# Kernel optimization log

Hardware: AMD Instinct MI355X
Metric: run time of the kernel (lower is better)

## Reference

```python
import jax, jax.numpy as jnp
import numpy as np

S, N, H = 1024, 64, 1024  # source len, batch, hidden_size
INPUT_SIZE = 1024         # attention projection dim (linear1/linear2 out)


def setup_inputs() -> dict:
    key = jax.random.key(0)
    ks = jax.random.split(key, 8)
    sc_h = 1.0 / np.sqrt(H)
    sc_i = 1.0 / np.sqrt(INPUT_SIZE)
    return {
        "out_e": jax.random.normal(ks[0], (S, N, H), dtype=jnp.float32),
        "hidden_d": jax.random.normal(ks[1], (1, N, H), dtype=jnp.float32),
        # torch Linear weights are [out_features, in_features]
        "W1": jax.random.uniform(ks[2], (INPUT_SIZE, H), jnp.float32, -sc_h, sc_h),
        "b1": jax.random.uniform(ks[3], (INPUT_SIZE,), jnp.float32, -sc_h, sc_h),
        "W2": jax.random.uniform(ks[4], (INPUT_SIZE, H), jnp.float32, -sc_h, sc_h),
        "b2": jax.random.uniform(ks[5], (INPUT_SIZE,), jnp.float32, -sc_h, sc_h),
        "W3": jax.random.uniform(ks[6], (1, INPUT_SIZE), jnp.float32, -sc_i, sc_i),
        "b3": jax.random.uniform(ks[7], (1,), jnp.float32, -sc_i, sc_i),
    }


def reference(out_e, hidden_d, W1, b1, W2, b2, W3, b3):
    # hidden_d [1,N,H] broadcast to [S,N,H] (torch .repeat)
    s = out_e.shape[0]
    hd = jnp.broadcast_to(hidden_d, (s,) + hidden_d.shape[1:])
    # a: [S,N,1] = linear3(tanh(linear1(hd) + linear2(out_e)))
    e = jnp.tanh(hd @ W1.T + b1 + out_e @ W2.T + b2)
    a = e @ W3.T + b3
    # softmax over the source dim (dim=0 in torch)
    alpha = jax.nn.softmax(a, axis=0)          # [S,N,1]
    c = jnp.einsum('sne,snh->enh', alpha, out_e)  # [1,N,H]
    return (c, alpha)
```

## Files before the change

### kernel.cpp

```cpp
#include <hip/hip_runtime.h>
#include <hip/hip_fp16.h>

#define S_LEN 1024
#define N_B   64
#define H_DIM 1024
#define I_DIM 1024

typedef __attribute__((ext_vector_type(8))) _Float16 half8;
typedef __attribute__((ext_vector_type(4))) _Float16 half4;
typedef __attribute__((ext_vector_type(4))) float    f32x4;

__device__ __forceinline__ void gload16(const void* g, void* l) {
  __builtin_amdgcn_global_load_lds(
      (const __attribute__((address_space(1))) unsigned int*)g,
      (__attribute__((address_space(3))) unsigned int*)l, 16, 0, 0);
}

__global__ __launch_bounds__(256) void setup_kernel(
    const float* __restrict__ out_e, const float* __restrict__ hd,
    const float* __restrict__ W1, const float* __restrict__ b1,
    const float* __restrict__ b2, const float* __restrict__ W2,
    _Float16* __restrict__ oe16, _Float16* __restrict__ w216,
    float* __restrict__ u1, float* __restrict__ a_ws,
    float* __restrict__ c_out) {
  __shared__ float hs[4 * 1024];
  const int bx = blockIdx.x;
  const int t = threadIdx.x;

  if (bx < 4096) {
    const float4* s4 = (const float4*)out_e;
    half8* d8 = (half8*)oe16;
    int i = bx * 256 + t;
#pragma unroll
    for (int r = 0; r < 8; ++r, i += 1048576) {
      float4 a = s4[2 * i], b = s4[2 * i + 1];
      half8 h;
      h[0] = (_Float16)a.x; h[1] = (_Float16)a.y;
      h[2] = (_Float16)a.z; h[3] = (_Float16)a.w;
      h[4] = (_Float16)b.x; h[5] = (_Float16)b.y;
      h[6] = (_Float16)b.z; h[7] = (_Float16)b.w;
      d8[i] = h;
    }
    return;
  }
  if (bx < 4160) {
    const float4* s4 = (const float4*)W2;
    half8* d8 = (half8*)w216;
    int i = (bx - 4096) * 256 + t;
#pragma unroll
    for (int r = 0; r < 8; ++r, i += 16384) {
      float4 a = s4[2 * i], b = s4[2 * i + 1];
      half8 h;
      h[0] = (_Float16)a.x; h[1] = (_Float16)a.y;
      h[2] = (_Float16)a.z; h[3] = (_Float16)a.w;
      h[4] = (_Float16)b.x; h[5] = (_Float16)b.y;
      h[6] = (_Float16)b.z; h[7] = (_Float16)b.w;
      d8[i] = h;
    }
    return;
  }
  const int local = bx - 4160;
  a_ws[local * 256 + t] = 0.f;
  c_out[local * 256 + t] = 0.f;

  const int nb = local & 15;
  const int ib = local >> 4;
  const int n0 = nb * 4;

  const float4* g4 = (const float4*)(hd + (size_t)n0 * 1024);
  float4* h4 = (float4*)hs;
#pragma unroll
  for (int r = 0; r < 4; ++r) h4[r * 256 + t] = g4[r * 256 + t];
  __syncthreads();

  int il = t >> 2, q = t & 3;
  int i = ib * 64 + il;
  const float4* w4 = (const float4*)(W1 + (size_t)i * 1024 + q * 256);
  float s0 = 0.f, s1 = 0.f, s2 = 0.f, s3 = 0.f;
  for (int hh = 0; hh < 64; ++hh) {
    float4 wv = w4[hh];
    int hb = q * 256 + hh * 4;
    float4 v0 = *(const float4*)&hs[0 * 1024 + hb];
    float4 v1 = *(const float4*)&hs[1 * 1024 + hb];
    float4 v2 = *(const float4*)&hs[2 * 1024 + hb];
    float4 v3 = *(const float4*)&hs[3 * 1024 + hb];
    s0 += wv.x * v0.x + wv.y * v0.y + wv.z * v0.z + wv.w * v0.w;
    s1 += wv.x * v1.x + wv.y * v1.y + wv.z * v1.z + wv.w * v1.w;
    s2 += wv.x * v2.x + wv.y * v2.y + wv.z * v2.z + wv.w * v2.w;
    s3 += wv.x * v3.x + wv.y * v3.y + wv.z * v3.z + wv.w * v3.w;
  }
  s0 += __shfl_xor(s0, 1); s0 += __shfl_xor(s0, 2);
  s1 += __shfl_xor(s1, 1); s1 += __shfl_xor(s1, 2);
  s2 += __shfl_xor(s2, 1); s2 += __shfl_xor(s2, 2);
  s3 += __shfl_xor(s3, 1); s3 += __shfl_xor(s3, 2);
  if (q == 0) {
    float bb = b1[i] + b2[i];
    u1[(size_t)(n0 + 0) * 1024 + i] = s0 + bb;
    u1[(size_t)(n0 + 1) * 1024 + i] = s1 + bb;
    u1[(size_t)(n0 + 2) * 1024 + i] = s2 + bb;
    u1[(size_t)(n0 + 3) * 1024 + i] = s3 + bb;
  }
}

__global__ __launch_bounds__(256) void fused_gemm_tanh(
    const _Float16* __restrict__ A,
    const _Float16* __restrict__ B,
    const float* __restrict__ u1,
    const float* __restrict__ W3,
    float* __restrict__ a_ws)
{
  __shared__ __align__(16) _Float16 As[2][128 * 32];
  __shared__ __align__(16) _Float16 Bs[2][128 * 32];

  const int t = threadIdx.x;
  const int lane = t & 63;
  const int w = t >> 6;
  const int wr = w >> 1, wc = w & 1;
  const int bx = blockIdx.x;
  const int xcd = bx & 7;
  const int j = bx >> 3;
  const int rb = xcd + ((j >> 3) << 3);
  const int cb = j & 7;
  const int m0 = rb * 128, i0 = cb * 128;

  const int strow = t >> 2;
  const int stcol = (t & 3) * 8;
  const _Float16* gA = A + (size_t)(m0 + strow) * 1024 + stcol;
  const _Float16* gB = B + (size_t)(i0 + strow) * 1024 + stcol;
  const int ldsoff = strow * 32 + stcol;

  f32x4 acc[4][4] = {};

  gload16(gA,             &As[0][ldsoff]);
  gload16(gA + 64 * 1024, &As[0][ldsoff + 64 * 32]);
  gload16(gB,             &Bs[0][ldsoff]);
  gload16(gB + 64 * 1024, &Bs[0][ldsoff + 64 * 32]);
  __syncthreads();

  const int fr = lane & 15;
  const int kg = lane >> 4;
  const int aoff = (wr * 64 + fr) * 32 + kg * 8;
  const int boff = (wc * 64 + fr) * 32 + kg * 8;

  for (int kt = 0; kt < 32; ++kt) {
    const int buf = kt & 1;
    if (kt < 31) {
      const _Float16* gA2 = gA + (kt + 1) * 32;
      const _Float16* gB2 = gB + (kt + 1) * 32;
      gload16(gA2,             &As[buf ^ 1][ldsoff]);
      gload16(gA2 + 64 * 1024, &As[buf ^ 1][ldsoff + 64 * 32]);
      gload16(gB2,             &Bs[buf ^ 1][ldsoff]);
      gload16(gB2 + 64 * 1024, &Bs[buf ^ 1][ldsoff + 64 * 32]);
    }
    half8 af[4], bf[4];
#pragma unroll
    for (int mi = 0; mi < 4; ++mi)
      af[mi] = *(const half8*)&As[buf][aoff + mi * 16 * 32];
#pragma unroll
    for (int ni = 0; ni < 4; ++ni)
      bf[ni] = *(const half8*)&Bs[buf][boff + ni * 16 * 32];
#pragma unroll
    for (int mi = 0; mi < 4; ++mi)
#pragma unroll
      for (int ni = 0; ni < 4; ++ni)
        acc[mi][ni] = __builtin_amdgcn_mfma_f32_16x16x32_f16(
            af[mi], bf[ni], acc[mi][ni], 0, 0, 0);
    __syncthreads();
  }

  float w3v[4];
#pragma unroll
  for (int ni = 0; ni < 4; ++ni)
    w3v[ni] = W3[i0 + wc * 64 + ni * 16 + fr];

#pragma unroll
  for (int mi = 0; mi < 4; ++mi) {
#pragma unroll
    for (int jj = 0; jj < 4; ++jj) {
      int m = m0 + wr * 64 + mi * 16 + kg * 4 + jj;
      int n = m & 63;
      const float* u1row = u1 + (size_t)n * 1024 + i0 + wc * 64;
      float s = 0.f;
#pragma unroll
      for (int ni = 0; ni < 4; ++ni) {
        float e = acc[mi][ni][jj] + u1row[ni * 16 + fr];
        float th = 1.f - 2.f / (__expf(2.f * e) + 1.f);
        s += th * w3v[ni];
      }
      s += __shfl_xor(s, 1);
      s += __shfl_xor(s, 2);
      s += __shfl_xor(s, 4);
      s += __shfl_xor(s, 8);
      if (fr == 0) atomicAdd(&a_ws[m], s);
    }
  }
}

__global__ __launch_bounds__(256) void softmax_wsum(
    const float* __restrict__ a_ws, const _Float16* __restrict__ oe,
    float* __restrict__ alpha, float* __restrict__ cout) {
  const int n = blockIdx.x & 63;
  const int sc = blockIdx.x >> 6;
  const int t = threadIdx.x;
  __shared__ float red[256];
  __shared__ float al[64];

  float v[4];
  float mx = -1e30f;
#pragma unroll
  for (int q = 0; q < 4; ++q) {
    v[q] = a_ws[(size_t)(t + q * 256) * 64 + n];
    mx = fmaxf(mx, v[q]);
  }
  red[t] = mx; __syncthreads();
  for (int off = 128; off > 0; off >>= 1) {
    if (t < off) red[t] = fmaxf(red[t], red[t + off]);
    __syncthreads();
  }
  mx = red[0];
  __syncthreads();
  float sum = 0.f;
#pragma unroll
  for (int q = 0; q < 4; ++q) { v[q] = __expf(v[q] - mx); sum += v[q]; }
  red[t] = sum; __syncthreads();
  for (int off = 128; off > 0; off >>= 1) {
    if (t < off) red[t] += red[t + off];
    __syncthreads();
  }
  const float inv = 1.f / red[0];

  const int q0 = sc >> 2;
  const int tlo = (sc & 3) * 64;
  if (t >= tlo && t < tlo + 64) {
    float a = v[q0] * inv;
    al[t - tlo] = a;
    alpha[(size_t)(sc * 64 + (t - tlo)) * 64 + n] = a;
  }
  __syncthreads();

  float a0 = 0.f, a1 = 0.f, a2 = 0.f, a3 = 0.f;
#pragma unroll 4
  for (int sl = 0; sl < 64; ++sl) {
    float a = al[sl];
    int s = sc * 64 + sl;
    half4 x = *(const half4*)(oe + (size_t)(s * 64 + n) * 1024 + t * 4);
    a0 += a * (float)x[0]; a1 += a * (float)x[1];
    a2 += a * (float)x[2]; a3 += a * (float)x[3];
  }
  float* c = cout + (size_t)n * 1024 + t * 4;
  atomicAdd(c + 0, a0);
  atomicAdd(c + 1, a1);
  atomicAdd(c + 2, a2);
  atomicAdd(c + 3, a3);
}

extern "C" void kernel_launch(void* const* d_in, const int* in_sizes, int n_in,
                              void* d_out, int out_size, void* d_ws,
                              size_t ws_size, hipStream_t stream) {
  const float* out_e    = (const float*)d_in[0];
  const float* hidden_d = (const float*)d_in[1];
  const float* W1       = (const float*)d_in[2];
  const float* b1       = (const float*)d_in[3];
  const float* W2       = (const float*)d_in[4];
  const float* b2       = (const float*)d_in[5];
  const float* W3       = (const float*)d_in[6];

  char* ws = (char*)d_ws;
  _Float16* oe16 = (_Float16*)ws;
  _Float16* w216 = (_Float16*)(ws + 134217728);
  float* u1   = (float*)(ws + 134217728 + 2097152);
  float* a_ws = (float*)(ws + 134217728 + 2097152 + 262144);

  float* c_out = (float*)d_out;
  float* alpha = (float*)d_out + 65536;

  hipLaunchKernelGGL(setup_kernel, dim3(4416), dim3(256), 0, stream,
                     out_e, hidden_d, W1, b1, b2, W2,
                     oe16, w216, u1, a_ws, c_out);
  hipLaunchKernelGGL(fused_gemm_tanh, dim3(4096), dim3(256), 0, stream,
                     oe16, w216, u1, W3, a_ws);
  hipLaunchKernelGGL(softmax_wsum, dim3(1024), dim3(256), 0, stream,
                     a_ws, oe16, alpha, c_out);
}
```

Baseline: 648.4 us.

## Enlarge GEMM tiles to 256x256 with 4-stage LDS pipeline and priority scheduling

```diff
diff --git a/kernel.cpp b/kernel.cpp
--- a/kernel.cpp
+++ b/kernel.cpp
@@ -102,88 +102,105 @@
   }
 }
 
-__global__ __launch_bounds__(256) void fused_gemm_tanh(
+__global__ __launch_bounds__(512, 2) void fused_gemm_tanh(
     const _Float16* __restrict__ A,
     const _Float16* __restrict__ B,
     const float* __restrict__ u1,
     const float* __restrict__ W3,
     float* __restrict__ a_ws)
 {
-  __shared__ __align__(16) _Float16 As[2][128 * 32];
-  __shared__ __align__(16) _Float16 Bs[2][128 * 32];
+  __shared__ __align__(16) _Float16 As[4][256 * 32];
+  __shared__ __align__(16) _Float16 Bs[4][256 * 32];
 
   const int t = threadIdx.x;
   const int lane = t & 63;
   const int w = t >> 6;
-  const int wr = w >> 1, wc = w & 1;
+  const int wr = w >> 2, wc = w & 3;
   const int bx = blockIdx.x;
   const int xcd = bx & 7;
   const int j = bx >> 3;
-  const int rb = xcd + ((j >> 3) << 3);
-  const int cb = j & 7;
-  const int m0 = rb * 128, i0 = cb * 128;
-
-  const int strow = t >> 2;
-  const int stcol = (t & 3) * 8;
-  const _Float16* gA = A + (size_t)(m0 + strow) * 1024 + stcol;
-  const _Float16* gB = B + (size_t)(i0 + strow) * 1024 + stcol;
-  const int ldsoff = strow * 32 + stcol;
-
-  f32x4 acc[4][4] = {};
-
-  gload16(gA,             &As[0][ldsoff]);
-  gload16(gA + 64 * 1024, &As[0][ldsoff + 64 * 32]);
-  gload16(gB,             &Bs[0][ldsoff]);
-  gload16(gB + 64 * 1024, &Bs[0][ldsoff + 64 * 32]);
-  __syncthreads();
+  const int rb = xcd + ((j >> 2) << 3);
+  const int cb = j & 3;
+  const int m0 = rb * 256, i0 = cb * 256;
 
   const int fr = lane & 15;
   const int kg = lane >> 4;
-  const int aoff = (wr * 64 + fr) * 32 + kg * 8;
+
+  const _Float16* gA0 = A + (size_t)(m0 + (t >> 2)) * 1024 + (t & 3) * 8;
+  const _Float16* gB0 = B + (size_t)(i0 + (t >> 2)) * 1024 + (t & 3) * 8;
+  const int ldst = t * 8;
+
+#define STAGE_A(kt) do { int b_ = (kt) & 3; int kc = (kt) * 32;      \
+    gload16(gA0 + kc,          &As[b_][ldst]);                        \
+    gload16(gA0 + kc + 131072, &As[b_][ldst + 4096]); } while (0)
+#define STAGE_B(kt) do { int b_ = (kt) & 3; int kc = (kt) * 32;      \
+    gload16(gB0 + kc,          &Bs[b_][ldst]);                        \
+    gload16(gB0 + kc + 131072, &Bs[b_][ldst + 4096]); } while (0)
+
+  f32x4 acc[8][4] = {};
+
+  STAGE_A(0); STAGE_B(0);
+  STAGE_A(1); STAGE_B(1);
+  STAGE_A(2); STAGE_B(2);
+
+  const int aoff = (wr * 128 + fr) * 32 + kg * 8;
   const int boff = (wc * 64 + fr) * 32 + kg * 8;
 
-  for (int kt = 0; kt < 32; ++kt) {
-    const int buf = kt & 1;
-    if (kt < 31) {
-      const _Float16* gA2 = gA + (kt + 1) * 32;
-      const _Float16* gB2 = gB + (kt + 1) * 32;
-      gload16(gA2,             &As[buf ^ 1][ldsoff]);
-      gload16(gA2 + 64 * 1024, &As[buf ^ 1][ldsoff + 64 * 32]);
-      gload16(gB2,             &Bs[buf ^ 1][ldsoff]);
-      gload16(gB2 + 64 * 1024, &Bs[buf ^ 1][ldsoff + 64 * 32]);
-    }
-    half8 af[4], bf[4];
-#pragma unroll
-    for (int mi = 0; mi < 4; ++mi)
-      af[mi] = *(const half8*)&As[buf][aoff + mi * 16 * 32];
-#pragma unroll
-    for (int ni = 0; ni < 4; ++ni)
-      bf[ni] = *(const half8*)&Bs[buf][boff + ni * 16 * 32];
-#pragma unroll
-    for (int mi = 0; mi < 4; ++mi)
-#pragma unroll
-      for (int ni = 0; ni < 4; ++ni)
-        acc[mi][ni] = __builtin_amdgcn_mfma_f32_16x16x32_f16(
-            af[mi], bf[ni], acc[mi][ni], 0, 0, 0);
-    __syncthreads();
-  }
+#define GATE(N) do {                                           \
+    asm volatile("s_waitcnt vmcnt(" #N ")" ::: "memory");      \
+    asm volatile("s_barrier" ::: "memory"); } while (0)
+
+#define PHASES(kt, DO_STAGE) do {                                         \
+    const _Float16* As_ = &As[(kt) & 3][0];                               \
+    const _Float16* Bs_ = &Bs[(kt) & 3][0];                               \
+    half8 bf[4], af[4];                                                   \
+    _Pragma("unroll") for (int ni = 0; ni < 4; ++ni)                      \
+      bf[ni] = *(const half8*)&Bs_[boff + ni * 512];                      \
+    _Pragma("unroll") for (int mi = 0; mi < 4; ++mi)                      \
+      af[mi] = *(const half8*)&As_[aoff + mi * 512];                      \
+    if (DO_STAGE) STAGE_A((kt) + 3);                                      \
+    __builtin_amdgcn_s_setprio(1);                                        \
+    _Pragma("unroll") for (int mi = 0; mi < 4; ++mi)                      \
+      _Pragma("unroll") for (int ni = 0; ni < 4; ++ni)                    \
+        acc[mi][ni] = __builtin_amdgcn_mfma_f32_16x16x32_f16(             \
+            af[mi], bf[ni], acc[mi][ni], 0, 0, 0);                        \
+    __builtin_amdgcn_s_setprio(0);                                        \
+    _Pragma("unroll") for (int mi = 0; mi < 4; ++mi)                      \
+      af[mi] = *(const half8*)&As_[aoff + (4 + mi) * 512];                \
+    if (DO_STAGE) STAGE_B((kt) + 3);                                      \
+    __builtin_amdgcn_s_setprio(1);                                        \
+    _Pragma("unroll") for (int mi = 0; mi < 4; ++mi)                      \
+      _Pragma("unroll") for (int ni = 0; ni < 4; ++ni)                    \
+        acc[4 + mi][ni] = __builtin_amdgcn_mfma_f32_16x16x32_f16(         \
+            af[mi], bf[ni], acc[4 + mi][ni], 0, 0, 0);                    \
+    __builtin_amdgcn_s_setprio(0); } while (0)
+
+  for (int kt = 0; kt < 29; ++kt) { GATE(8); PHASES(kt, 1); }
+  GATE(8); PHASES(29, 0);
+  GATE(4); PHASES(30, 0);
+  GATE(0); PHASES(31, 0);
+
+#undef PHASES
+#undef GATE
+#undef STAGE_A
+#undef STAGE_B
 
   float w3v[4];
 #pragma unroll
   for (int ni = 0; ni < 4; ++ni)
     w3v[ni] = W3[i0 + wc * 64 + ni * 16 + fr];
-
-#pragma unroll
-  for (int mi = 0; mi < 4; ++mi) {
+  const float* u1base = u1 + i0 + wc * 64 + fr;
+
+#pragma unroll
+  for (int mi = 0; mi < 8; ++mi) {
 #pragma unroll
     for (int jj = 0; jj < 4; ++jj) {
-      int m = m0 + wr * 64 + mi * 16 + kg * 4 + jj;
-      int n = m & 63;
-      const float* u1row = u1 + (size_t)n * 1024 + i0 + wc * 64;
+      int m = m0 + wr * 128 + mi * 16 + kg * 4 + jj;
+      const float* u1row = u1base + (size_t)(m & 63) * 1024;
       float s = 0.f;
 #pragma unroll
       for (int ni = 0; ni < 4; ++ni) {
-        float e = acc[mi][ni][jj] + u1row[ni * 16 + fr];
+        float e = acc[mi][ni][jj] + u1row[ni * 16];
         float th = 1.f - 2.f / (__expf(2.f * e) + 1.f);
         s += th * w3v[ni];
       }
@@ -277,7 +294,7 @@
   hipLaunchKernelGGL(setup_kernel, dim3(4416), dim3(256), 0, stream,
                      out_e, hidden_d, W1, b1, b2, W2,
                      oe16, w216, u1, a_ws, c_out);
-  hipLaunchKernelGGL(fused_gemm_tanh, dim3(4096), dim3(256), 0, stream,
+  hipLaunchKernelGGL(fused_gemm_tanh, dim3(1024), dim3(512), 0, stream,
                      oe16, w216, u1, W3, a_ws);
   hipLaunchKernelGGL(softmax_wsum, dim3(1024), dim3(256), 0, stream,
                      a_ws, oe16, alpha, c_out);
```

Measured after the change: 635.0 us. 2.1% less time.
